# Optimization experiments

Measured on AMD Instinct MI355X. Metric: run time of the kernel, lower is better.

Reference implementation:

```python
import jax, jax.numpy as jnp
import numpy as np

N_BITS = 8
N_LEVELS = 2 ** N_BITS  # 256
MAX_ITERS = 10
BIG = 3.0e38  # stand-in for +inf that stays finite in fp32


def _init_scales(x):
    """Replicates init_quantization_scale: iteratively peel off 3-sigma outliers.
    Returns per-iteration (thresholds, deltas, zero_points, valid) arrays of
    length MAX_ITERS; `valid[i]` marks iterations that actually recorded a group
    (torch's `break` on empty non-zero set)."""
    xf = x.reshape(-1)

    def step(carry, _):
        xc, done = carry
        absx = jnp.abs(xc)
        nz = xc != 0.0
        n = jnp.sum(nz)
        active = jnp.logical_and(jnp.logical_not(done), n > 0)
        nf = jnp.maximum(n, 1).astype(xc.dtype)
        # mean / unbiased variance of |non-zero elements| (torch .mean()/.var())
        mean = jnp.sum(jnp.where(nz, absx, 0.0)) / nf
        var = jnp.sum(jnp.where(nz, (absx - mean) ** 2, 0.0)) / jnp.maximum(nf - 1.0, 1.0)
        thr = mean + 3.0 * jnp.sqrt(var)
        max_abs = jnp.max(absx)
        # if thr > max: inliers = non-zero elements; else inliers = ~outliers (zeros included)
        inlier = jnp.where(thr > max_abs, nz, absx <= thr)
        x_min = jnp.min(jnp.where(inlier, xc, jnp.asarray(BIG, xc.dtype)))
        x_max = jnp.max(jnp.where(inlier, xc, jnp.asarray(-BIG, xc.dtype)))
        delta = (x_max - x_min) / (N_LEVELS - 1)
        zp = jnp.round(-x_min / delta)
        # keep only outliers for the next iteration
        xc_next = jnp.where(active, jnp.where(absx > thr, xc, 0.0), xc)
        done_next = jnp.logical_or(done, n == 0)
        return (xc_next, done_next), (thr, delta, zp, active)

    (_, _), (thrs, deltas, zps, valids) = jax.lax.scan(
        step, (xf, jnp.asarray(False)), None, length=MAX_ITERS)
    return thrs, deltas, zps, valids


def _dequant(x, thrs, deltas, zps, valids):
    absx = jnp.abs(x)
    # group index: band i is (thr[i-1], thr[i]]; band 0 contributes 0 as in torch
    gi = jnp.zeros(x.shape, dtype=jnp.int32)
    for i in range(1, MAX_ITERS):  # static, small loop over groups
        band = (absx > thrs[i - 1]) & (absx <= thrs[i]) & valids[i]
        gi = gi + band.astype(jnp.int32) * i
    n_groups = jnp.sum(valids.astype(jnp.int32))
    gi = jnp.clip(gi, 0, jnp.maximum(n_groups - 1, 0))
    d = deltas[gi]   # per-element scale
    z = zps[gi]      # per-element zero point
    x_q = jnp.clip(jnp.round(x / d) + z, 0.0, float(N_LEVELS - 1))
    return (x_q - z) * d


def setup_inputs() -> dict:
    key = jax.random.key(0)
    x = jax.random.normal(key, (4, 4096, 4096), dtype=jnp.float32)
    return {"x": x}


def reference(x):
    thrs, deltas, zps, valids = _init_scales(x)
    return _dequant(x, thrs, deltas, zps, valids)
```

## Files before the change

kernel.cpp:

```cpp
#include <hip/hip_runtime.h>

#define BIGF 3.402823466e38f
#define LCAP 2048u
#define NB   2048
#define NT   256

struct State {
  double sum0, sumsq0;
  double sum1, sumsq1;
  double sum2, sumsq2;
  unsigned n0, n1, n2;
  float maxabs0, minnz0, maxnz0;
  float maxabs1, minnz1, maxnz1;
  float maxabs2, minnz2, maxnz2;
  float bmin0, bmax0;
  float bmin1, bmax1;
  unsigned count1, count2;
  float thr0f, thr1f;
  int special0;
  float thr[10], delta[10], zp[10];
  int valid[10];
};

__device__ inline void atomicMinF(float* addr, float v) {
  unsigned* ua = (unsigned*)addr;
  unsigned cur = *ua;
  while (v < __uint_as_float(cur)) {
    unsigned prev = atomicCAS(ua, cur, __float_as_uint(v));
    if (prev == cur) break;
    cur = prev;
  }
}
__device__ inline void atomicMaxF(float* addr, float v) {
  unsigned* ua = (unsigned*)addr;
  unsigned cur = *ua;
  while (v > __uint_as_float(cur)) {
    unsigned prev = atomicCAS(ua, cur, __float_as_uint(v));
    if (prev == cur) break;
    cur = prev;
  }
}

struct Acc8 {
  double sum, sumsq;
  unsigned cnt;
  float maxabs, minnz, maxnz, bmin, bmax;
};
__device__ inline void acc_init(Acc8& a) {
  a.sum = 0.0; a.sumsq = 0.0; a.cnt = 0u;
  a.maxabs = 0.0f;
  a.minnz = BIGF; a.maxnz = -BIGF;
  a.bmin = BIGF; a.bmax = -BIGF;
}
__device__ inline void acc_merge(Acc8& a, const Acc8& b) {
  a.sum += b.sum; a.sumsq += b.sumsq; a.cnt += b.cnt;
  a.maxabs = fmaxf(a.maxabs, b.maxabs);
  a.minnz = fminf(a.minnz, b.minnz); a.maxnz = fmaxf(a.maxnz, b.maxnz);
  a.bmin = fminf(a.bmin, b.bmin);   a.bmax = fmaxf(a.bmax, b.bmax);
}
__device__ inline void acc_wave_reduce(Acc8& a) {
  #pragma unroll
  for (int off = 32; off > 0; off >>= 1) {
    a.sum    += __shfl_down(a.sum, off);
    a.sumsq  += __shfl_down(a.sumsq, off);
    a.cnt    += __shfl_down(a.cnt, off);
    a.maxabs = fmaxf(a.maxabs, __shfl_down(a.maxabs, off));
    a.minnz  = fminf(a.minnz,  __shfl_down(a.minnz, off));
    a.maxnz  = fmaxf(a.maxnz,  __shfl_down(a.maxnz, off));
    a.bmin   = fminf(a.bmin,   __shfl_down(a.bmin, off));
    a.bmax   = fmaxf(a.bmax,   __shfl_down(a.bmax, off));
  }
}
template <int NWAVES>
__device__ inline bool acc_block_reduce(Acc8& a, Acc8* s_part) {
  __syncthreads();
  acc_wave_reduce(a);
  int tid = threadIdx.x;
  if ((tid & 63) == 0) s_part[tid >> 6] = a;
  __syncthreads();
  if (tid == 0) {
    #pragma unroll
    for (int w = 1; w < NWAVES; ++w) acc_merge(a, s_part[w]);
    return true;
  }
  return false;
}

__device__ inline float compute_thr(double sum, double sumsq, unsigned n) {
  double nf = (double)(n > 0u ? n : 1u);
  double mean = sum / nf;
  double nm1 = nf - 1.0; if (nm1 < 1.0) nm1 = 1.0;
  double var = (sumsq - sum * sum / nf) / nm1;
  if (var < 0.0) var = 0.0;
  return (float)(mean + 3.0 * sqrt(var));
}

__device__ inline void finalize_group(float thr, float maxabs, unsigned n,
                                      float minnz, float maxnz, float bmin, float bmax,
                                      bool clampZero, float* dOut, float* zOut, int* vOut) {
  float xmin, xmax;
  if (thr > maxabs) { xmin = minnz; xmax = maxnz; }
  else {
    xmin = bmin; xmax = bmax;
    if (clampZero) { xmin = fminf(xmin, 0.0f); xmax = fmaxf(xmax, 0.0f); }
  }
  float d = (xmax - xmin) / 255.0f;
  int v = (n > 0u) ? 1 : 0;
  float z;
  if (v && d > 0.0f && d < BIGF) { z = rintf((-xmin) / d); }
  else { d = 1.0f; z = 0.0f; }
  *dOut = d; *zOut = z; *vOut = v;
}

__global__ void k0_init(State* st) {
  if (threadIdx.x == 0 && blockIdx.x == 0) {
    st->sum0 = 0.0; st->sumsq0 = 0.0; st->n0 = 0u;
    st->maxabs0 = 0.0f; st->minnz0 = BIGF; st->maxnz0 = -BIGF;
    st->sum1 = 0.0; st->sumsq1 = 0.0; st->n1 = 0u;
    st->maxabs1 = 0.0f; st->minnz1 = BIGF; st->maxnz1 = -BIGF;
    st->sum2 = 0.0; st->sumsq2 = 0.0; st->n2 = 0u;
    st->maxabs2 = 0.0f; st->minnz2 = BIGF; st->maxnz2 = -BIGF;
    st->bmin0 = BIGF; st->bmax0 = -BIGF;
    st->bmin1 = BIGF; st->bmax1 = -BIGF;
    st->count1 = 0u; st->count2 = 0u;
  }
}

__device__ inline void stat1(float f, Acc8& a) {
  float ab = fabsf(f);
  bool nz = (f != 0.0f);
  a.cnt += nz ? 1u : 0u;
  double dab = (double)ab;
  a.sum += dab; a.sumsq += dab * dab;
  a.maxabs = fmaxf(a.maxabs, ab);
  a.minnz = fminf(a.minnz, nz ? f : BIGF);
  a.maxnz = fmaxf(a.maxnz, nz ? f : -BIGF);
}

__global__ void __launch_bounds__(256) k1_stats(const float* __restrict__ x, long long n,
                                                Acc8* __restrict__ part) {
  __shared__ Acc8 s_part[4];
  Acc8 a0, a1; acc_init(a0); acc_init(a1);
  const float4* x4 = (const float4*)x;
  long long n4 = n >> 2;
  long long tid = (long long)blockIdx.x * NT + threadIdx.x;
  long long nthreads = (long long)gridDim.x * NT;
  long long step = nthreads * 4;
  long long nfull = (n4 / step) * step;
  for (long long i = (long long)blockIdx.x * (NT * 4) + threadIdx.x; i < nfull; i += step) {
    float4 v0 = x4[i];
    float4 v1 = x4[i + NT];
    float4 v2 = x4[i + 2 * NT];
    float4 v3 = x4[i + 3 * NT];
    stat1(v0.x, a0); stat1(v0.y, a0); stat1(v0.z, a0); stat1(v0.w, a0);
    stat1(v1.x, a0); stat1(v1.y, a0); stat1(v1.z, a0); stat1(v1.w, a0);
    stat1(v2.x, a1); stat1(v2.y, a1); stat1(v2.z, a1); stat1(v2.w, a1);
    stat1(v3.x, a1); stat1(v3.y, a1); stat1(v3.z, a1); stat1(v3.w, a1);
  }
  for (long long i = nfull + tid; i < n4; i += nthreads) {
    float4 v = x4[i];
    stat1(v.x, a0); stat1(v.y, a0); stat1(v.z, a0); stat1(v.w, a0);
  }
  for (long long i = (n4 << 2) + tid; i < n; i += nthreads) stat1(x[i], a0);

  acc_merge(a0, a1);
  if (acc_block_reduce<4>(a0, s_part)) part[blockIdx.x] = a0;
}

__global__ void __launch_bounds__(1024) k1r_reduce(State* st, const Acc8* __restrict__ part, int np) {
  __shared__ Acc8 s_part[16];
  Acc8 a; acc_init(a);
  for (int j = threadIdx.x; j < np; j += 1024) acc_merge(a, part[j]);
  if (acc_block_reduce<16>(a, s_part)) {
    st->sum0 = a.sum; st->sumsq0 = a.sumsq; st->n0 = a.cnt;
    st->maxabs0 = a.maxabs; st->minnz0 = a.minnz; st->maxnz0 = a.maxnz;
    float t = compute_thr(a.sum, a.sumsq, a.cnt);
    st->thr0f = t;
    st->special0 = (t > a.maxabs) ? 1 : 0;
  }
}

__device__ inline void proc2(float f, float thr0, bool special, Acc8& a,
                             unsigned* l_cnt, float* l_buf,
                             State* st, float* __restrict__ buf1, unsigned cap1) {
  float ab = fabsf(f);
  bool out = ab > thr0;
  bool inl = special ? (f != 0.0f) : (!out);
  a.bmin = fminf(a.bmin, inl ? f : BIGF);
  a.bmax = fmaxf(a.bmax, inl ? f : -BIGF);
  a.cnt += out ? 1u : 0u;
  double dab = out ? (double)ab : 0.0;
  a.sum += dab; a.sumsq += dab * dab;
  a.maxabs = fmaxf(a.maxabs, out ? ab : 0.0f);
  a.minnz = fminf(a.minnz, out ? f : BIGF);
  a.maxnz = fmaxf(a.maxnz, out ? f : -BIGF);
  unsigned long long m = __ballot(out);
  if (m) {
    unsigned lo = (unsigned)m, hi = (unsigned)(m >> 32);
    int pw = (int)__builtin_amdgcn_mbcnt_hi(hi, __builtin_amdgcn_mbcnt_lo(lo, 0u));
    int nout = __builtin_popcountll(m);
    int leader = __builtin_ctzll(m);
    unsigned bbase = 0u;
    if ((int)(threadIdx.x & 63) == leader) bbase = atomicAdd(l_cnt, (unsigned)nout);
    bbase = (unsigned)__shfl((int)bbase, leader);
    if (out) {
      unsigned p = bbase + (unsigned)pw;
      if (p < LCAP) l_buf[p] = f;
      else { unsigned g = atomicAdd(&st->count1, 1u); if (g < cap1) buf1[g] = f; }
    }
  }
}

__global__ void __launch_bounds__(256) k2_pass(const float* __restrict__ x, long long n, State* st,
                                               float* __restrict__ buf1, unsigned cap1,
                                               Acc8* __restrict__ part) {
  __shared__ Acc8 s_part[4];
  __shared__ float l_buf[LCAP];
  __shared__ unsigned l_cnt, l_base, l_m;
  if (threadIdx.x == 0) l_cnt = 0u;
  __syncthreads();

  float thr0 = st->thr0f;
  bool special = st->special0 != 0;

  Acc8 a0, a1; acc_init(a0); acc_init(a1);
  const float4* x4 = (const float4*)x;
  long long n4 = n >> 2;
  long long tid = (long long)blockIdx.x * NT + threadIdx.x;
  long long nthreads = (long long)gridDim.x * NT;
  long long step = nthreads * 4;
  long long nfull = (n4 / step) * step;
  for (long long i = (long long)blockIdx.x * (NT * 4) + threadIdx.x; i < nfull; i += step) {
    float4 v0 = x4[i];
    float4 v1 = x4[i + NT];
    float4 v2 = x4[i + 2 * NT];
    float4 v3 = x4[i + 3 * NT];
    proc2(v0.x, thr0, special, a0, &l_cnt, l_buf, st, buf1, cap1);
    proc2(v0.y, thr0, special, a0, &l_cnt, l_buf, st, buf1, cap1);
    proc2(v0.z, thr0, special, a0, &l_cnt, l_buf, st, buf1, cap1);
    proc2(v0.w, thr0, special, a0, &l_cnt, l_buf, st, buf1, cap1);
    proc2(v1.x, thr0, special, a0, &l_cnt, l_buf, st, buf1, cap1);
    proc2(v1.y, thr0, special, a0, &l_cnt, l_buf, st, buf1, cap1);
    proc2(v1.z, thr0, special, a0, &l_cnt, l_buf, st, buf1, cap1);
    proc2(v1.w, thr0, special, a0, &l_cnt, l_buf, st, buf1, cap1);
    proc2(v2.x, thr0, special, a1, &l_cnt, l_buf, st, buf1, cap1);
    proc2(v2.y, thr0, special, a1, &l_cnt, l_buf, st, buf1, cap1);
    proc2(v2.z, thr0, special, a1, &l_cnt, l_buf, st, buf1, cap1);
    proc2(v2.w, thr0, special, a1, &l_cnt, l_buf, st, buf1, cap1);
    proc2(v3.x, thr0, special, a1, &l_cnt, l_buf, st, buf1, cap1);
    proc2(v3.y, thr0, special, a1, &l_cnt, l_buf, st, buf1, cap1);
    proc2(v3.z, thr0, special, a1, &l_cnt, l_buf, st, buf1, cap1);
    proc2(v3.w, thr0, special, a1, &l_cnt, l_buf, st, buf1, cap1);
  }
  for (long long i = nfull + tid; i < n4; i += nthreads) {
    float4 v = x4[i];
    proc2(v.x, thr0, special, a0, &l_cnt, l_buf, st, buf1, cap1);
    proc2(v.y, thr0, special, a0, &l_cnt, l_buf, st, buf1, cap1);
    proc2(v.z, thr0, special, a0, &l_cnt, l_buf, st, buf1, cap1);
    proc2(v.w, thr0, special, a0, &l_cnt, l_buf, st, buf1, cap1);
  }
  for (long long i = (n4 << 2) + tid; i < n; i += nthreads) {
    proc2(x[i], thr0, special, a0, &l_cnt, l_buf, st, buf1, cap1);
  }

  __syncthreads();
  if (threadIdx.x == 0) {
    l_m = l_cnt < LCAP ? l_cnt : LCAP;
    l_base = atomicAdd(&st->count1, l_m);
  }
  __syncthreads();
  for (unsigned i = threadIdx.x; i < l_m; i += NT) {
    unsigned g = l_base + i;
    if (g < cap1) buf1[g] = l_buf[i];
  }
  acc_merge(a0, a1);
  if (acc_block_reduce<4>(a0, s_part)) part[blockIdx.x] = a0;
}

__global__ void __launch_bounds__(1024) k2r_reduce(State* st, const Acc8* __restrict__ part, int np) {
  __shared__ Acc8 s_part[16];
  Acc8 a; acc_init(a);
  for (int j = threadIdx.x; j < np; j += 1024) acc_merge(a, part[j]);
  if (acc_block_reduce<16>(a, s_part)) {
    st->bmin0 = a.bmin; st->bmax0 = a.bmax;
    st->sum1 = a.sum; st->sumsq1 = a.sumsq; st->n1 = a.cnt;
    st->maxabs1 = a.maxabs; st->minnz1 = a.minnz; st->maxnz1 = a.maxnz;
    st->thr1f = compute_thr(a.sum, a.sumsq, a.cnt);
  }
}

__global__ void __launch_bounds__(256) k3_pass(State* st, const float* __restrict__ buf1, unsigned cap1,
                                               float* __restrict__ buf2, unsigned cap2) {
  __shared__ Acc8 s_part[4];
  __shared__ float l_buf[LCAP];
  __shared__ unsigned l_cnt, l_base, l_m;
  if (threadIdx.x == 0) l_cnt = 0u;
  __syncthreads();

  unsigned c1 = st->count1; if (c1 > cap1) c1 = cap1;
  float thr1 = st->thr1f;

  Acc8 a; acc_init(a);
  unsigned stride = gridDim.x * blockDim.x;
  for (unsigned j = blockIdx.x * blockDim.x + threadIdx.x; j < c1; j += stride) {
    float f = buf1[j];
    float ab = fabsf(f);
    if (ab <= thr1) { a.bmin = fminf(a.bmin, f); a.bmax = fmaxf(a.bmax, f); }
    else {
      a.cnt++; a.sum += (double)ab; a.sumsq += (double)ab * (double)ab;
      a.maxabs = fmaxf(a.maxabs, ab);
      a.minnz = fminf(a.minnz, f); a.maxnz = fmaxf(a.maxnz, f);
      unsigned p = atomicAdd(&l_cnt, 1u);
      if (p < LCAP) l_buf[p] = f;
      else { unsigned g = atomicAdd(&st->count2, 1u); if (g < cap2) buf2[g] = f; }
    }
  }
  __syncthreads();
  if (threadIdx.x == 0) {
    l_m = l_cnt < LCAP ? l_cnt : LCAP;
    l_base = atomicAdd(&st->count2, l_m);
  }
  __syncthreads();
  for (unsigned i = threadIdx.x; i < l_m; i += blockDim.x) {
    unsigned g = l_base + i;
    if (g < cap2) buf2[g] = l_buf[i];
  }
  if (acc_block_reduce<4>(a, s_part)) {
    atomicMinF(&st->bmin1, a.bmin); atomicMaxF(&st->bmax1, a.bmax);
    atomicAdd(&st->sum2, a.sum); atomicAdd(&st->sumsq2, a.sumsq); atomicAdd(&st->n2, a.cnt);
    atomicMaxF(&st->maxabs2, a.maxabs);
    atomicMinF(&st->minnz2, a.minnz); atomicMaxF(&st->maxnz2, a.maxnz);
  }
}

__global__ void __launch_bounds__(1024) k4_finalize(State* st, const float* __restrict__ buf2, unsigned cap2) {
  __shared__ Acc8 s_part[16];
  __shared__ float sh_thr[10], sh_delta[10], sh_zp[10];
  __shared__ int sh_valid[10];
  __shared__ double sh_sum, sh_sumsq;
  __shared__ unsigned sh_n;
  __shared__ float sh_maxabs, sh_minnz, sh_maxnz;
  int tid = threadIdx.x;

  if (tid == 0) {
    float thr0 = compute_thr(st->sum0, st->sumsq0, st->n0);
    sh_thr[0] = thr0;
    finalize_group(thr0, st->maxabs0, st->n0, st->minnz0, st->maxnz0,
                   st->bmin0, st->bmax0, false,
                   &sh_delta[0], &sh_zp[0], &sh_valid[0]);
    float thr1 = compute_thr(st->sum1, st->sumsq1, st->n1);
    sh_thr[1] = thr1;
    finalize_group(thr1, st->maxabs1, st->n1, st->minnz1, st->maxnz1,
                   st->bmin1, st->bmax1, true,
                   &sh_delta[1], &sh_zp[1], &sh_valid[1]);
    sh_sum = st->sum2; sh_sumsq = st->sumsq2; sh_n = st->n2;
    sh_maxabs = st->maxabs2; sh_minnz = st->minnz2; sh_maxnz = st->maxnz2;
  }
  __syncthreads();
  unsigned c2 = st->count2; if (c2 > cap2) c2 = cap2;

  for (int i = 2; i < 10; ++i) {
    if (tid == 0) sh_thr[i] = compute_thr(sh_sum, sh_sumsq, sh_n);
    __syncthreads();
    float tp = sh_thr[i - 1], tc = sh_thr[i];
    Acc8 a; acc_init(a);
    for (unsigned j = tid; j < c2; j += 1024u) {
      float f = buf2[j];
      float ab = fabsf(f);
      if (ab > tp && ab <= tc) { a.bmin = fminf(a.bmin, f); a.bmax = fmaxf(a.bmax, f); }
      if (ab > tc) {
        a.cnt++; a.sum += (double)ab; a.sumsq += (double)ab * (double)ab;
        a.maxabs = fmaxf(a.maxabs, ab);
        a.minnz = fminf(a.minnz, f); a.maxnz = fmaxf(a.maxnz, f);
      }
    }
    if (acc_block_reduce<16>(a, s_part)) {
      finalize_group(tc, sh_maxabs, sh_n, sh_minnz, sh_maxnz, a.bmin, a.bmax,
                     true, &sh_delta[i], &sh_zp[i], &sh_valid[i]);
      if (sh_n > 0u) {
        sh_sum = a.sum; sh_sumsq = a.sumsq; sh_n = a.cnt;
        sh_maxabs = a.maxabs; sh_minnz = a.minnz; sh_maxnz = a.maxnz;
      }
    }
    __syncthreads();
  }
  if (tid < 10) {
    st->thr[tid] = sh_thr[tid]; st->delta[tid] = sh_delta[tid];
    st->zp[tid] = sh_zp[tid];   st->valid[tid] = sh_valid[tid];
  }
}

__device__ inline float dq1(float v, const float* thr, const float* dl, const float* zp, const int* vld) {
  float ab = fabsf(v);
  float d = dl[0], z = zp[0];
  #pragma unroll
  for (int i = 1; i < 10; ++i) {
    bool band = (vld[i] != 0) && (ab > thr[i - 1]) && (ab <= thr[i]);
    d = band ? dl[i] : d;
    z = band ? zp[i] : z;
  }
  float q = rintf(v / d) + z;
  q = fminf(fmaxf(q, 0.0f), 255.0f);
  return (q - z) * d;
}
__device__ inline float4 dq4(float4 v, const float* thr, const float* dl, const float* zp, const int* vld) {
  float4 o;
  o.x = dq1(v.x, thr, dl, zp, vld);
  o.y = dq1(v.y, thr, dl, zp, vld);
  o.z = dq1(v.z, thr, dl, zp, vld);
  o.w = dq1(v.w, thr, dl, zp, vld);
  return o;
}

__global__ void __launch_bounds__(256) k5_dequant(const float* __restrict__ x, float* __restrict__ out,
                                                  long long n, const State* __restrict__ st) {
  float thr[10], dl[10], zp[10]; int vld[10];
  #pragma unroll
  for (int i = 0; i < 10; ++i) {
    thr[i] = st->thr[i]; dl[i] = st->delta[i]; zp[i] = st->zp[i]; vld[i] = st->valid[i];
  }
  const float4* x4 = (const float4*)x;
  float4* o4 = (float4*)out;
  long long n4 = n >> 2;
  long long tid = (long long)blockIdx.x * NT + threadIdx.x;
  long long nthreads = (long long)gridDim.x * NT;
  long long step = nthreads * 4;
  long long nfull = (n4 / step) * step;
  for (long long i = (long long)blockIdx.x * (NT * 4) + threadIdx.x; i < nfull; i += step) {
    float4 v0 = x4[i];
    float4 v1 = x4[i + NT];
    float4 v2 = x4[i + 2 * NT];
    float4 v3 = x4[i + 3 * NT];
    o4[i]          = dq4(v0, thr, dl, zp, vld);
    o4[i + NT]     = dq4(v1, thr, dl, zp, vld);
    o4[i + 2 * NT] = dq4(v2, thr, dl, zp, vld);
    o4[i + 3 * NT] = dq4(v3, thr, dl, zp, vld);
  }
  for (long long i = nfull + tid; i < n4; i += nthreads) {
    o4[i] = dq4(x4[i], thr, dl, zp, vld);
  }
  for (long long i = (n4 << 2) + tid; i < n; i += nthreads) {
    out[i] = dq1(x[i], thr, dl, zp, vld);
  }
}

extern "C" void kernel_launch(void* const* d_in, const int* in_sizes, int n_in,
                              void* d_out, int out_size, void* d_ws, size_t ws_size,
                              hipStream_t stream) {
  const float* x = (const float*)d_in[0];
  float* out = (float*)d_out;
  long long n = (long long)in_sizes[0];

  char* p = (char*)d_ws;
  State* st = (State*)p;            p += 4096;
  Acc8* part1 = (Acc8*)p;           p += (size_t)NB * sizeof(Acc8);
  Acc8* part2 = (Acc8*)p;           p += (size_t)NB * sizeof(Acc8);
  size_t used = (size_t)(p - (char*)d_ws);
  used = (used + 255) & ~(size_t)255;
  size_t avail = ws_size > used ? ws_size - used : 0;
  size_t cap2_sz = avail / 8;
  if (cap2_sz > (size_t)(1u << 20) * 4) cap2_sz = (size_t)(1u << 20) * 4;
  unsigned cap2 = (unsigned)(cap2_sz / 4);
  float* buf2 = (float*)((char*)d_ws + used);
  float* buf1 = buf2 + cap2;
  unsigned cap1 = (unsigned)((avail - (size_t)cap2 * 4) / 4);

  hipLaunchKernelGGL(k0_init,     dim3(1),   dim3(64),   0, stream, st);
  hipLaunchKernelGGL(k1_stats,    dim3(NB),  dim3(NT),   0, stream, x, n, part1);
  hipLaunchKernelGGL(k1r_reduce,  dim3(1),   dim3(1024), 0, stream, st, (const Acc8*)part1, NB);
  hipLaunchKernelGGL(k2_pass,     dim3(NB),  dim3(NT),   0, stream, x, n, st, buf1, cap1, part2);
  hipLaunchKernelGGL(k2r_reduce,  dim3(1),   dim3(1024), 0, stream, st, (const Acc8*)part2, NB);
  hipLaunchKernelGGL(k3_pass,     dim3(256), dim3(NT),   0, stream, st, buf1, cap1, buf2, cap2);
  hipLaunchKernelGGL(k4_finalize, dim3(1),   dim3(1024), 0, stream, st, buf2, cap2);
  hipLaunchKernelGGL(k5_dequant,  dim3(NB),  dim3(NT),   0, stream, x, out, n, st);
}
```

Before: 704.3 us.

## Dequantize bulk with group-0 scale and scatter-fix outliers separately

The outlier compaction buffer now stores each outlier's value together with its flat index. The main dequant kernel then applies only the group-0 scale to every element, and a new small kernel rewrites the outlier positions with the full band lookup. This removes the per-element 10-way band selection from the bandwidth-bound pass. Other changes fold the init kernel into the first reduce, drop redundant maxabs tracking, unroll the stats pass 8-wide, and use nontemporal stores. The cost is twice the outlier buffer size and a 32-bit index that limits tensor size, plus an extra launch.

New measurement: 676.6 us. 3.9% less time.

```diff
diff --git a/kernel.cpp b/kernel.cpp
--- a/kernel.cpp
+++ b/kernel.cpp
@@ -4,6 +4,8 @@
 #define LCAP 2048u
 #define NB   2048
 #define NT   256
+
+typedef float f32x4 __attribute__((ext_vector_type(4)));
 
 struct State {
   double sum0, sumsq0;
@@ -112,20 +114,6 @@
   *dOut = d; *zOut = z; *vOut = v;
 }
 
-__global__ void k0_init(State* st) {
-  if (threadIdx.x == 0 && blockIdx.x == 0) {
-    st->sum0 = 0.0; st->sumsq0 = 0.0; st->n0 = 0u;
-    st->maxabs0 = 0.0f; st->minnz0 = BIGF; st->maxnz0 = -BIGF;
-    st->sum1 = 0.0; st->sumsq1 = 0.0; st->n1 = 0u;
-    st->maxabs1 = 0.0f; st->minnz1 = BIGF; st->maxnz1 = -BIGF;
-    st->sum2 = 0.0; st->sumsq2 = 0.0; st->n2 = 0u;
-    st->maxabs2 = 0.0f; st->minnz2 = BIGF; st->maxnz2 = -BIGF;
-    st->bmin0 = BIGF; st->bmax0 = -BIGF;
-    st->bmin1 = BIGF; st->bmax1 = -BIGF;
-    st->count1 = 0u; st->count2 = 0u;
-  }
-}
-
 __device__ inline void stat1(float f, Acc8& a) {
   float ab = fabsf(f);
   bool nz = (f != 0.0f);
@@ -140,31 +128,33 @@
 __global__ void __launch_bounds__(256) k1_stats(const float* __restrict__ x, long long n,
                                                 Acc8* __restrict__ part) {
   __shared__ Acc8 s_part[4];
-  Acc8 a0, a1; acc_init(a0); acc_init(a1);
-  const float4* x4 = (const float4*)x;
+  Acc8 a[4];
+  #pragma unroll
+  for (int u = 0; u < 4; ++u) acc_init(a[u]);
+  const f32x4* x4 = (const f32x4*)x;
   long long n4 = n >> 2;
   long long tid = (long long)blockIdx.x * NT + threadIdx.x;
   long long nthreads = (long long)gridDim.x * NT;
-  long long step = nthreads * 4;
+  long long step = nthreads * 8;
   long long nfull = (n4 / step) * step;
-  for (long long i = (long long)blockIdx.x * (NT * 4) + threadIdx.x; i < nfull; i += step) {
-    float4 v0 = x4[i];
-    float4 v1 = x4[i + NT];
-    float4 v2 = x4[i + 2 * NT];
-    float4 v3 = x4[i + 3 * NT];
-    stat1(v0.x, a0); stat1(v0.y, a0); stat1(v0.z, a0); stat1(v0.w, a0);
-    stat1(v1.x, a0); stat1(v1.y, a0); stat1(v1.z, a0); stat1(v1.w, a0);
-    stat1(v2.x, a1); stat1(v2.y, a1); stat1(v2.z, a1); stat1(v2.w, a1);
-    stat1(v3.x, a1); stat1(v3.y, a1); stat1(v3.z, a1); stat1(v3.w, a1);
+  for (long long i = (long long)blockIdx.x * (NT * 8) + threadIdx.x; i < nfull; i += step) {
+    f32x4 v[8];
+    #pragma unroll
+    for (int u = 0; u < 8; ++u) v[u] = x4[i + u * NT];
+    #pragma unroll
+    for (int u = 0; u < 8; ++u) {
+      stat1(v[u].x, a[u & 3]); stat1(v[u].y, a[u & 3]);
+      stat1(v[u].z, a[u & 3]); stat1(v[u].w, a[u & 3]);
+    }
   }
   for (long long i = nfull + tid; i < n4; i += nthreads) {
-    float4 v = x4[i];
-    stat1(v.x, a0); stat1(v.y, a0); stat1(v.z, a0); stat1(v.w, a0);
-  }
-  for (long long i = (n4 << 2) + tid; i < n; i += nthreads) stat1(x[i], a0);
-
-  acc_merge(a0, a1);
-  if (acc_block_reduce<4>(a0, s_part)) part[blockIdx.x] = a0;
+    f32x4 v = x4[i];
+    stat1(v.x, a[0]); stat1(v.y, a[0]); stat1(v.z, a[0]); stat1(v.w, a[0]);
+  }
+  for (long long i = (n4 << 2) + tid; i < n; i += nthreads) stat1(x[i], a[0]);
+
+  acc_merge(a[0], a[1]); acc_merge(a[2], a[3]); acc_merge(a[0], a[2]);
+  if (acc_block_reduce<4>(a[0], s_part)) part[blockIdx.x] = a[0];
 }
 
 __global__ void __launch_bounds__(1024) k1r_reduce(State* st, const Acc8* __restrict__ part, int np) {
@@ -177,12 +167,16 @@
     float t = compute_thr(a.sum, a.sumsq, a.cnt);
     st->thr0f = t;
     st->special0 = (t > a.maxabs) ? 1 : 0;
-  }
-}
-
-__device__ inline void proc2(float f, float thr0, bool special, Acc8& a,
-                             unsigned* l_cnt, float* l_buf,
-                             State* st, float* __restrict__ buf1, unsigned cap1) {
+    st->count1 = 0u; st->count2 = 0u;
+    st->bmin1 = BIGF; st->bmax1 = -BIGF;
+    st->sum2 = 0.0; st->sumsq2 = 0.0; st->n2 = 0u;
+    st->maxabs2 = a.maxabs; st->minnz2 = BIGF; st->maxnz2 = -BIGF;
+  }
+}
+
+__device__ inline void proc2(float f, unsigned idx, float thr0, bool special, Acc8& a,
+                             unsigned* l_cnt, float2* l_buf,
+                             State* st, float2* __restrict__ buf1, unsigned cap1) {
   float ab = fabsf(f);
   bool out = ab > thr0;
   bool inl = special ? (f != 0.0f) : (!out);
@@ -191,7 +185,6 @@
   a.cnt += out ? 1u : 0u;
   double dab = out ? (double)ab : 0.0;
   a.sum += dab; a.sumsq += dab * dab;
-  a.maxabs = fmaxf(a.maxabs, out ? ab : 0.0f);
   a.minnz = fminf(a.minnz, out ? f : BIGF);
   a.maxnz = fmaxf(a.maxnz, out ? f : -BIGF);
   unsigned long long m = __ballot(out);
@@ -205,17 +198,18 @@
     bbase = (unsigned)__shfl((int)bbase, leader);
     if (out) {
       unsigned p = bbase + (unsigned)pw;
-      if (p < LCAP) l_buf[p] = f;
-      else { unsigned g = atomicAdd(&st->count1, 1u); if (g < cap1) buf1[g] = f; }
+      float2 rec = make_float2(f, __uint_as_float(idx));
+      if (p < LCAP) l_buf[p] = rec;
+      else { unsigned g = atomicAdd(&st->count1, 1u); if (g < cap1) buf1[g] = rec; }
     }
   }
 }
 
 __global__ void __launch_bounds__(256) k2_pass(const float* __restrict__ x, long long n, State* st,
-                                               float* __restrict__ buf1, unsigned cap1,
+                                               float2* __restrict__ buf1, unsigned cap1,
                                                Acc8* __restrict__ part) {
   __shared__ Acc8 s_part[4];
-  __shared__ float l_buf[LCAP];
+  __shared__ float2 l_buf[LCAP];
   __shared__ unsigned l_cnt, l_base, l_m;
   if (threadIdx.x == 0) l_cnt = 0u;
   __syncthreads();
@@ -224,43 +218,46 @@
   bool special = st->special0 != 0;
 
   Acc8 a0, a1; acc_init(a0); acc_init(a1);
-  const float4* x4 = (const float4*)x;
+  const f32x4* x4 = (const f32x4*)x;
   long long n4 = n >> 2;
   long long tid = (long long)blockIdx.x * NT + threadIdx.x;
   long long nthreads = (long long)gridDim.x * NT;
   long long step = nthreads * 4;
   long long nfull = (n4 / step) * step;
   for (long long i = (long long)blockIdx.x * (NT * 4) + threadIdx.x; i < nfull; i += step) {
-    float4 v0 = x4[i];
-    float4 v1 = x4[i + NT];
-    float4 v2 = x4[i + 2 * NT];
-    float4 v3 = x4[i + 3 * NT];
-    proc2(v0.x, thr0, special, a0, &l_cnt, l_buf, st, buf1, cap1);
-    proc2(v0.y, thr0, special, a0, &l_cnt, l_buf, st, buf1, cap1);
-    proc2(v0.z, thr0, special, a0, &l_cnt, l_buf, st, buf1, cap1);
-    proc2(v0.w, thr0, special, a0, &l_cnt, l_buf, st, buf1, cap1);
-    proc2(v1.x, thr0, special, a0, &l_cnt, l_buf, st, buf1, cap1);
-    proc2(v1.y, thr0, special, a0, &l_cnt, l_buf, st, buf1, cap1);
-    proc2(v1.z, thr0, special, a0, &l_cnt, l_buf, st, buf1, cap1);
-    proc2(v1.w, thr0, special, a0, &l_cnt, l_buf, st, buf1, cap1);
-    proc2(v2.x, thr0, special, a1, &l_cnt, l_buf, st, buf1, cap1);
-    proc2(v2.y, thr0, special, a1, &l_cnt, l_buf, st, buf1, cap1);
-    proc2(v2.z, thr0, special, a1, &l_cnt, l_buf, st, buf1, cap1);
-    proc2(v2.w, thr0, special, a1, &l_cnt, l_buf, st, buf1, cap1);
-    proc2(v3.x, thr0, special, a1, &l_cnt, l_buf, st, buf1, cap1);
-    proc2(v3.y, thr0, special, a1, &l_cnt, l_buf, st, buf1, cap1);
-    proc2(v3.z, thr0, special, a1, &l_cnt, l_buf, st, buf1, cap1);
-    proc2(v3.w, thr0, special, a1, &l_cnt, l_buf, st, buf1, cap1);
+    f32x4 v0 = x4[i];
+    f32x4 v1 = x4[i + NT];
+    f32x4 v2 = x4[i + 2 * NT];
+    f32x4 v3 = x4[i + 3 * NT];
+    unsigned b0 = (unsigned)(i) << 2, b1 = (unsigned)(i + NT) << 2,
+             b2 = (unsigned)(i + 2 * NT) << 2, b3 = (unsigned)(i + 3 * NT) << 2;
+    proc2(v0.x, b0 + 0u, thr0, special, a0, &l_cnt, l_buf, st, buf1, cap1);
+    proc2(v0.y, b0 + 1u, thr0, special, a0, &l_cnt, l_buf, st, buf1, cap1);
+    proc2(v0.z, b0 + 2u, thr0, special, a0, &l_cnt, l_buf, st, buf1, cap1);
+    proc2(v0.w, b0 + 3u, thr0, special, a0, &l_cnt, l_buf, st, buf1, cap1);
+    proc2(v1.x, b1 + 0u, thr0, special, a0, &l_cnt, l_buf, st, buf1, cap1);
+    proc2(v1.y, b1 + 1u, thr0, special, a0, &l_cnt, l_buf, st, buf1, cap1);
+    proc2(v1.z, b1 + 2u, thr0, special, a0, &l_cnt, l_buf, st, buf1, cap1);
+    proc2(v1.w, b1 + 3u, thr0, special, a0, &l_cnt, l_buf, st, buf1, cap1);
+    proc2(v2.x, b2 + 0u, thr0, special, a1, &l_cnt, l_buf, st, buf1, cap1);
+    proc2(v2.y, b2 + 1u, thr0, special, a1, &l_cnt, l_buf, st, buf1, cap1);
+    proc2(v2.z, b2 + 2u, thr0, special, a1, &l_cnt, l_buf, st, buf1, cap1);
+    proc2(v2.w, b2 + 3u, thr0, special, a1, &l_cnt, l_buf, st, buf1, cap1);
+    proc2(v3.x, b3 + 0u, thr0, special, a1, &l_cnt, l_buf, st, buf1, cap1);
+    proc2(v3.y, b3 + 1u, thr0, special, a1, &l_cnt, l_buf, st, buf1, cap1);
+    proc2(v3.z, b3 + 2u, thr0, special, a1, &l_cnt, l_buf, st, buf1, cap1);
+    proc2(v3.w, b3 + 3u, thr0, special, a1, &l_cnt, l_buf, st, buf1, cap1);
   }
   for (long long i = nfull + tid; i < n4; i += nthreads) {
-    float4 v = x4[i];
-    proc2(v.x, thr0, special, a0, &l_cnt, l_buf, st, buf1, cap1);
-    proc2(v.y, thr0, special, a0, &l_cnt, l_buf, st, buf1, cap1);
-    proc2(v.z, thr0, special, a0, &l_cnt, l_buf, st, buf1, cap1);
-    proc2(v.w, thr0, special, a0, &l_cnt, l_buf, st, buf1, cap1);
+    f32x4 v = x4[i];
+    unsigned b = (unsigned)(i) << 2;
+    proc2(v.x, b + 0u, thr0, special, a0, &l_cnt, l_buf, st, buf1, cap1);
+    proc2(v.y, b + 1u, thr0, special, a0, &l_cnt, l_buf, st, buf1, cap1);
+    proc2(v.z, b + 2u, thr0, special, a0, &l_cnt, l_buf, st, buf1, cap1);
+    proc2(v.w, b + 3u, thr0, special, a0, &l_cnt, l_buf, st, buf1, cap1);
   }
   for (long long i = (n4 << 2) + tid; i < n; i += nthreads) {
-    proc2(x[i], thr0, special, a0, &l_cnt, l_buf, st, buf1, cap1);
+    proc2(x[i], (unsigned)i, thr0, special, a0, &l_cnt, l_buf, st, buf1, cap1);
   }
 
   __syncthreads();
@@ -284,12 +281,13 @@
   if (acc_block_reduce<16>(a, s_part)) {
     st->bmin0 = a.bmin; st->bmax0 = a.bmax;
     st->sum1 = a.sum; st->sumsq1 = a.sumsq; st->n1 = a.cnt;
-    st->maxabs1 = a.maxabs; st->minnz1 = a.minnz; st->maxnz1 = a.maxnz;
+    st->maxabs1 = st->maxabs0;
+    st->minnz1 = a.minnz; st->maxnz1 = a.maxnz;
     st->thr1f = compute_thr(a.sum, a.sumsq, a.cnt);
   }
 }
 
-__global__ void __launch_bounds__(256) k3_pass(State* st, const float* __restrict__ buf1, unsigned cap1,
+__global__ void __launch_bounds__(256) k3_pass(State* st, const float2* __restrict__ buf1, unsigned cap1,
                                                float* __restrict__ buf2, unsigned cap2) {
   __shared__ Acc8 s_part[4];
   __shared__ float l_buf[LCAP];
@@ -303,12 +301,11 @@
   Acc8 a; acc_init(a);
   unsigned stride = gridDim.x * blockDim.x;
   for (unsigned j = blockIdx.x * blockDim.x + threadIdx.x; j < c1; j += stride) {
-    float f = buf1[j];
+    float f = buf1[j].x;
     float ab = fabsf(f);
     if (ab <= thr1) { a.bmin = fminf(a.bmin, f); a.bmax = fmaxf(a.bmax, f); }
     else {
       a.cnt++; a.sum += (double)ab; a.sumsq += (double)ab * (double)ab;
-      a.maxabs = fmaxf(a.maxabs, ab);
       a.minnz = fminf(a.minnz, f); a.maxnz = fmaxf(a.maxnz, f);
       unsigned p = atomicAdd(&l_cnt, 1u);
       if (p < LCAP) l_buf[p] = f;
@@ -328,7 +325,6 @@
   if (acc_block_reduce<4>(a, s_part)) {
     atomicMinF(&st->bmin1, a.bmin); atomicMaxF(&st->bmax1, a.bmax);
     atomicAdd(&st->sum2, a.sum); atomicAdd(&st->sumsq2, a.sumsq); atomicAdd(&st->n2, a.cnt);
-    atomicMaxF(&st->maxabs2, a.maxabs);
     atomicMinF(&st->minnz2, a.minnz); atomicMaxF(&st->maxnz2, a.maxnz);
   }
 }
@@ -390,6 +386,48 @@
   }
 }
 
+__device__ inline float dq0(float v, float d0, float z0) {
+  float q = rintf(v / d0) + z0;
+  q = fminf(fmaxf(q, 0.0f), 255.0f);
+  return (q - z0) * d0;
+}
+
+__global__ void __launch_bounds__(256) k5_dequant(const float* __restrict__ x, float* __restrict__ out,
+                                                  long long n, const State* __restrict__ st) {
+  float d0 = st->delta[0], z0 = st->zp[0];
+  const f32x4* x4 = (const f32x4*)x;
+  f32x4* o4 = (f32x4*)out;
+  long long n4 = n >> 2;
+  long long tid = (long long)blockIdx.x * NT + threadIdx.x;
+  long long nthreads = (long long)gridDim.x * NT;
+  long long step = nthreads * 8;
+  long long nfull = (n4 / step) * step;
+  for (long long i = (long long)blockIdx.x * (NT * 8) + threadIdx.x; i < nfull; i += step) {
+    f32x4 v[8];
+    #pragma unroll
+    for (int u = 0; u < 8; ++u) v[u] = x4[i + u * NT];
+    #pragma unroll
+    for (int u = 0; u < 8; ++u) {
+      f32x4 o;
+      o.x = dq0(v[u].x, d0, z0);
+      o.y = dq0(v[u].y, d0, z0);
+      o.z = dq0(v[u].z, d0, z0);
+      o.w = dq0(v[u].w, d0, z0);
+      __builtin_nontemporal_store(o, &o4[i + u * NT]);
+    }
+  }
+  for (long long i = nfull + tid; i < n4; i += nthreads) {
+    f32x4 v = x4[i];
+    f32x4 o;
+    o.x = dq0(v.x, d0, z0); o.y = dq0(v.y, d0, z0);
+    o.z = dq0(v.z, d0, z0); o.w = dq0(v.w, d0, z0);
+    o4[i] = o;
+  }
+  for (long long i = (n4 << 2) + tid; i < n; i += nthreads) {
+    out[i] = dq0(x[i], d0, z0);
+  }
+}
+
 __device__ inline float dq1(float v, const float* thr, const float* dl, const float* zp, const int* vld) {
   float ab = fabsf(v);
   float d = dl[0], z = zp[0];
@@ -403,44 +441,19 @@
   q = fminf(fmaxf(q, 0.0f), 255.0f);
   return (q - z) * d;
 }
-__device__ inline float4 dq4(float4 v, const float* thr, const float* dl, const float* zp, const int* vld) {
-  float4 o;
-  o.x = dq1(v.x, thr, dl, zp, vld);
-  o.y = dq1(v.y, thr, dl, zp, vld);
-  o.z = dq1(v.z, thr, dl, zp, vld);
-  o.w = dq1(v.w, thr, dl, zp, vld);
-  return o;
-}
-
-__global__ void __launch_bounds__(256) k5_dequant(const float* __restrict__ x, float* __restrict__ out,
-                                                  long long n, const State* __restrict__ st) {
+
+__global__ void __launch_bounds__(256) k6_outliers(const float2* __restrict__ buf1, unsigned cap1,
+                                                   float* __restrict__ out, const State* __restrict__ st) {
+  unsigned c1 = st->count1; if (c1 > cap1) c1 = cap1;
   float thr[10], dl[10], zp[10]; int vld[10];
   #pragma unroll
   for (int i = 0; i < 10; ++i) {
     thr[i] = st->thr[i]; dl[i] = st->delta[i]; zp[i] = st->zp[i]; vld[i] = st->valid[i];
   }
-  const float4* x4 = (const float4*)x;
-  float4* o4 = (float4*)out;
-  long long n4 = n >> 2;
-  long long tid = (long long)blockIdx.x * NT + threadIdx.x;
-  long long nthreads = (long long)gridDim.x * NT;
-  long long step = nthreads * 4;
-  long long nfull = (n4 / step) * step;
-  for (long long i = (long long)blockIdx.x * (NT * 4) + threadIdx.x; i < nfull; i += step) {
-    float4 v0 = x4[i];
-    float4 v1 = x4[i + NT];
-    float4 v2 = x4[i + 2 * NT];
-    float4 v3 = x4[i + 3 * NT];
-    o4[i]          = dq4(v0, thr, dl, zp, vld);
-    o4[i + NT]     = dq4(v1, thr, dl, zp, vld);
-    o4[i + 2 * NT] = dq4(v2, thr, dl, zp, vld);
-    o4[i + 3 * NT] = dq4(v3, thr, dl, zp, vld);
-  }
-  for (long long i = nfull + tid; i < n4; i += nthreads) {
-    o4[i] = dq4(x4[i], thr, dl, zp, vld);
-  }
-  for (long long i = (n4 << 2) + tid; i < n; i += nthreads) {
-    out[i] = dq1(x[i], thr, dl, zp, vld);
+  unsigned stride = gridDim.x * blockDim.x;
+  for (unsigned j = blockIdx.x * blockDim.x + threadIdx.x; j < c1; j += stride) {
+    float2 rec = buf1[j];
+    out[__float_as_uint(rec.y)] = dq1(rec.x, thr, dl, zp, vld);
   }
 }
 
@@ -462,15 +475,15 @@
   if (cap2_sz > (size_t)(1u << 20) * 4) cap2_sz = (size_t)(1u << 20) * 4;
   unsigned cap2 = (unsigned)(cap2_sz / 4);
   float* buf2 = (float*)((char*)d_ws + used);
-  float* buf1 = buf2 + cap2;
-  unsigned cap1 = (unsigned)((avail - (size_t)cap2 * 4) / 4);
-
-  hipLaunchKernelGGL(k0_init,     dim3(1),   dim3(64),   0, stream, st);
+  float2* buf1 = (float2*)(buf2 + cap2);
+  unsigned cap1 = (unsigned)((avail - (size_t)cap2 * 4) / 8);
+
   hipLaunchKernelGGL(k1_stats,    dim3(NB),  dim3(NT),   0, stream, x, n, part1);
   hipLaunchKernelGGL(k1r_reduce,  dim3(1),   dim3(1024), 0, stream, st, (const Acc8*)part1, NB);
   hipLaunchKernelGGL(k2_pass,     dim3(NB),  dim3(NT),   0, stream, x, n, st, buf1, cap1, part2);
   hipLaunchKernelGGL(k2r_reduce,  dim3(1),   dim3(1024), 0, stream, st, (const Acc8*)part2, NB);
-  hipLaunchKernelGGL(k3_pass,     dim3(256), dim3(NT),   0, stream, st, buf1, cap1, buf2, cap2);
-  hipLaunchKernelGGL(k4_finalize, dim3(1),   dim3(1024), 0, stream, st, buf2, cap2);
+  hipLaunchKernelGGL(k3_pass,     dim3(256), dim3(NT),   0, stream, st, (const float2*)buf1, cap1, buf2, cap2);
+  hipLaunchKernelGGL(k4_finalize, dim3(1),   dim3(1024), 0, stream, st, (const float*)buf2, cap2);
   hipLaunchKernelGGL(k5_dequant,  dim3(NB),  dim3(NT),   0, stream, x, out, n, st);
-}
+  hipLaunchKernelGGL(k6_outliers, dim3(512), dim3(NT),   0, stream, (const float2*)buf1, cap1, out, st);
+}
```
